# Kernel tuning notes

Hardware: AMD Instinct MI355X
Metric: run time of the kernel (lower is better)

## Reference

```python
import jax, jax.numpy as jnp
import numpy as np

B, R, IMG_DIM, TAG_DIM = 256, 36, 2048, 768
BOX_LEN = 15
POS_EMBED = 200
POS_SIZE = 16 * 16 + 1  # 257
EMBED_SIZE = 1024
EPS_NORM = 1e-8
EPS_ATTN = 1e-6


def setup_inputs() -> dict:
    key = jax.random.key(0)
    ks = jax.random.split(key, 8)
    images = jax.random.normal(ks[0], (B, R, IMG_DIM), dtype=jnp.float32)
    images_tag = jax.random.normal(ks[1], (B, R, TAG_DIM), dtype=jnp.float32)
    # boxes: first 15 entries are integer position indices, last 15 are weights
    box_idx = jax.random.randint(ks[2], (B, R, BOX_LEN), 0, POS_SIZE).astype(jnp.float32)
    box_w = jax.random.uniform(ks[3], (B, R, BOX_LEN), dtype=jnp.float32)
    boxes = jnp.concatenate([box_idx, box_w], axis=-1)  # [B,R,30]
    # parameters (xavier-uniform-like for linears, normal for embedding)
    pos_emb = jax.random.normal(ks[4], (POS_SIZE, POS_EMBED), dtype=jnp.float32)
    fan = (IMG_DIM + TAG_DIM) + POS_EMBED
    r1 = np.sqrt(6.0) / np.sqrt(fan)
    attn_W = jax.random.uniform(ks[5], (POS_EMBED, IMG_DIM + TAG_DIM), dtype=jnp.float32, minval=-r1, maxval=r1)
    fc_in = IMG_DIM + POS_EMBED + TAG_DIM
    r2 = np.sqrt(6.0) / np.sqrt(fc_in + EMBED_SIZE)
    fc_W = jax.random.uniform(ks[6], (EMBED_SIZE, fc_in), dtype=jnp.float32, minval=-r2, maxval=r2)
    fc_b = jnp.zeros((EMBED_SIZE,), dtype=jnp.float32)
    return {"images": images, "images_tag": images_tag, "boxes": boxes,
            "pos_emb": pos_emb, "attn_W": attn_W, "fc_W": fc_W, "fc_b": fc_b}


def reference(images, images_tag, boxes, pos_emb, attn_W, fc_W, fc_b):
    half = boxes.shape[2] // 2  # 15
    idx = boxes[..., :half].astype(jnp.int32)        # [B,R,15] position indices
    box_w = boxes[..., half:]                        # [B,R,15] weights
    img_tag = jnp.concatenate([images, images_tag], axis=-1)  # [B,R,2816]
    box_emb = pos_emb[idx]                           # [B,R,15,200]
    # posi_attn (vectorized over batch instead of python loop)
    region = jnp.einsum('brd,ed->bre', img_tag, attn_W)        # [B,R,200]
    scores = jnp.einsum('bre,brke->brk', region, box_emb)      # [B,R,15]
    attn = jax.nn.softmax(jnp.tanh(scores), axis=-1)
    attn = attn * box_w
    attn = attn / (jnp.sum(attn, axis=-1, keepdims=True) + EPS_ATTN)
    box_feat = jnp.einsum('brk,brke->bre', attn, box_emb)      # [B,R,200]
    # original uses .data -> detached attention output
    box_feat = jax.lax.stop_gradient(box_feat)
    image_position = jnp.concatenate([images, box_feat, images_tag], axis=-1)  # [B,R,3016]
    features = jnp.einsum('brd,ed->bre', image_position, fc_W) + fc_b
    norm = jnp.sqrt(jnp.sum(features ** 2, axis=-1, keepdims=True)) + EPS_NORM
    return features / norm
```

## Files before the change

### kernel.cpp

```cpp
#include <hip/hip_runtime.h>


#define M_TOT 9216
#define K1    2816
#define K2    3072
#define ES    1024

typedef __attribute__((ext_vector_type(8))) short bf16x8;
typedef __attribute__((ext_vector_type(4))) float floatx4;

static __device__ __forceinline__ unsigned short f2bf(float f) {
    unsigned int u = __float_as_uint(f);
    u += 0x7fffu + ((u >> 16) & 1u);
    return (unsigned short)(u >> 16);
}

static __device__ __forceinline__ void cvt8(const float* __restrict__ g,
                                            unsigned short* __restrict__ d) {
    const float4 f0 = *(const float4*)g;
    const float4 f1 = *(const float4*)(g + 4);
    uint4 pk;
    pk.x = (unsigned)f2bf(f0.x) | ((unsigned)f2bf(f0.y) << 16);
    pk.y = (unsigned)f2bf(f0.z) | ((unsigned)f2bf(f0.w) << 16);
    pk.z = (unsigned)f2bf(f1.x) | ((unsigned)f2bf(f1.y) << 16);
    pk.w = (unsigned)f2bf(f1.z) | ((unsigned)f2bf(f1.w) << 16);
    *(uint4*)d = pk;
}

static __device__ __forceinline__ void gl16(const void* g, const void* l) {
    __builtin_amdgcn_global_load_lds(
        (const __attribute__((address_space(1))) unsigned int*)g,
        (__attribute__((address_space(3))) unsigned int*)(unsigned int)(unsigned long long)l,
        16, 0, 0);
}

__global__ __launch_bounds__(384) void k_prep_a(
    const float* __restrict__ images,
    const float* __restrict__ tag,
    unsigned short* __restrict__ Abf)
{
    const int m = blockIdx.x;
    const int t = threadIdx.x;
    unsigned short* dst = Abf + (long)m * K2;
    if (t < 256) {
        cvt8(images + (long)m * 2048 + t * 8, dst + t * 8);
    } else if (t < 352) {
        const int j = t - 256;
        cvt8(tag + (long)m * 768 + j * 8, dst + 2304 + j * 8);
    }
}

__global__ __launch_bounds__(256) void k_prep_w(
    const float* __restrict__ attn_W,
    const float* __restrict__ fc_W,
    unsigned short* __restrict__ Wa,
    unsigned short* __restrict__ Wf)
{
    const int u = blockIdx.x * 256 + threadIdx.x;
    uint4 z; z.x = z.y = z.z = z.w = 0u;
    if (blockIdx.y == 0) {
        if (u < 208 * 352) {
            const int r = u / 352;
            const int c = (u - r * 352) * 8;
            if (r < 200) cvt8(attn_W + (long)r * K1 + c, Wa + (long)r * K1 + c);
            else         *(uint4*)(Wa + (long)r * K1 + c) = z;
        }
    } else {
        if (u < 1024 * 384) {
            const int r = u / 384;
            const int dc = (u - r * 384) * 8;
            unsigned short* d = Wf + (long)r * K2 + dc;
            if (dc < 2248)      cvt8(fc_W + (long)r * 3016 + dc, d);
            else if (dc < 2304) *(uint4*)d = z;
            else                cvt8(fc_W + (long)r * 3016 + (dc - 56), d);
        }
    }
}

__global__ __launch_bounds__(256, 2) void k_gemm1_attn(
    const unsigned short* __restrict__ Abf,
    const unsigned short* __restrict__ Wa,
    const float* __restrict__ boxes,
    const float* __restrict__ pos_emb,
    unsigned short* __restrict__ AbfBox)
{
    __shared__ __align__(16) unsigned short lds[14336];
    unsigned short* ldsA = lds;
    unsigned short* ldsB = lds + 1024;
    float* ldsR = (float*)lds;

    const int t = threadIdx.x;
    const int lane = t & 63;
    const int w = t >> 6;
    const int quad = lane >> 4;
    const int ln15 = lane & 15;
    const int x7 = ln15 & 7;
    const int m0 = blockIdx.x * 16;
    const int lrow = lane >> 3;
    const int schunk = (lane & 7) ^ lrow;
    const int nj = (w == 0) ? 4 : 3;

    floatx4 acc[4] = {};

    for (int kt = 0; kt < 44; ++kt) {
        const int kb = kt * 64;
        const int acol = kb + ((kb >= 2048) ? 256 : 0);
#pragma unroll
        for (int i = 0; i < 7; ++i) {
            const int u = w + i * 4;
            if (u < 26) {
                const int r = u * 8 + lrow;
                gl16(Wa + (long)r * K1 + kb + schunk * 8, ldsB + u * 512);
            } else {
                const int r = (u - 26) * 8 + lrow;
                gl16(Abf + (long)(m0 + r) * K2 + acol + schunk * 8,
                     ldsA + (u - 26) * 512);
            }
        }
        __syncthreads();
#pragma unroll
        for (int s = 0; s < 2; ++s) {
            const int g = s * 4 + quad;
            const int co = (g ^ x7) << 3;
            const bf16x8 a = *(const bf16x8*)&ldsA[ln15 * 64 + co];
#pragma unroll
            for (int jj = 0; jj < 4; ++jj) {
                if (jj < nj) {
                    const int j = w + jj * 4;
                    const bf16x8 b = *(const bf16x8*)&ldsB[(j * 16 + ln15) * 64 + co];
                    acc[jj] = __builtin_amdgcn_mfma_f32_16x16x32_bf16(a, b, acc[jj], 0, 0, 0);
                }
            }
        }
        __syncthreads();
    }

#pragma unroll
    for (int jj = 0; jj < 4; ++jj) {
        if (jj < nj) {
            const int j = w + jj * 4;
#pragma unroll
            for (int r = 0; r < 4; ++r)
                ldsR[(quad * 4 + r) * 212 + j * 16 + ln15] = acc[jj][r];
        }
    }
    __syncthreads();

    for (int rr = 0; rr < 4; ++rr) {
        const int ml = w * 4 + rr;
        const int m = m0 + ml;
        float rv[4];
#pragma unroll
        for (int c = 0; c < 4; ++c) {
            const int e = lane + c * 64;
            rv[c] = (e < 200) ? ldsR[ml * 212 + e] : 0.0f;
        }
        const float* bx = boxes + (long)m * 30;
        int idx[15]; float bw[15], sc[15];
#pragma unroll
        for (int k = 0; k < 15; ++k) {
            int ii = (int)bx[k];
            idx[k] = (ii < 0) ? 0 : (ii > 256 ? 256 : ii);
            bw[k] = bx[15 + k];
        }
#pragma unroll
        for (int k = 0; k < 15; ++k) {
            const float* em = pos_emb + (long)idx[k] * 200;
            float p = 0.0f;
#pragma unroll
            for (int c = 0; c < 4; ++c) {
                const int e = lane + c * 64;
                if (e < 200) p += rv[c] * em[e];
            }
            for (int off = 32; off; off >>= 1) p += __shfl_xor(p, off, 64);
            sc[k] = p;
        }
        float mx = -1e30f;
#pragma unroll
        for (int k = 0; k < 15; ++k) { sc[k] = tanhf(sc[k]); mx = fmaxf(mx, sc[k]); }
        float Z = 0.0f, den = 0.0f, pk[15];
#pragma unroll
        for (int k = 0; k < 15; ++k) { pk[k] = __expf(sc[k] - mx); Z += pk[k]; }
#pragma unroll
        for (int k = 0; k < 15; ++k) { pk[k] *= bw[k]; den += pk[k]; }
        den += 1e-6f * Z;
        const float inv = 1.0f / den;
        unsigned short* bo = AbfBox + (long)m * K2 + 2048;
#pragma unroll
        for (int c = 0; c < 4; ++c) {
            const int e = lane + c * 64;
            float o = 0.0f;
            if (e < 200) {
#pragma unroll
                for (int k = 0; k < 15; ++k) o += pk[k] * pos_emb[(long)idx[k] * 200 + e];
                o *= inv;
            }
            bo[e] = f2bf(o);
        }
    }
}

__global__ __launch_bounds__(256, 2) void k_gemm2(
    const unsigned short* __restrict__ Abf,
    const unsigned short* __restrict__ Wf,
    float* __restrict__ dout)
{
    __shared__ __align__(16) unsigned short ldsA[128 * 64];
    __shared__ __align__(16) unsigned short ldsB[128 * 64];
    const int t = threadIdx.x;
    const int lane = t & 63;
    const int w = t >> 6;
    const int quad = lane >> 4;
    const int ln15 = lane & 15;
    const int x7 = ln15 & 7;
    const int nx = blockIdx.x & 7;
    const int mx = blockIdx.x >> 3;
    const int m0 = mx * 128;
    const int n0 = nx * 128;
    const int lrow = lane >> 3;
    const int schunk = (lane & 7) ^ lrow;
    const int wm = (w & 1) * 64;
    const int wn = (w >> 1) * 64;

    floatx4 acc[4][4] = {};

    for (int kt = 0; kt < 48; ++kt) {
        const int kb = kt * 64;
#pragma unroll
        for (int i = 0; i < 4; ++i) {
            const int u = w * 4 + i;
            const int r = u * 8 + lrow;
            gl16(Abf + (long)(m0 + r) * K2 + kb + schunk * 8, ldsA + u * 512);
            gl16(Wf  + (long)(n0 + r) * K2 + kb + schunk * 8, ldsB + u * 512);
        }
        __syncthreads();
#pragma unroll
        for (int s = 0; s < 2; ++s) {
            const int g = s * 4 + quad;
            const int co = (g ^ x7) << 3;
            bf16x8 a[4], b[4];
#pragma unroll
            for (int i = 0; i < 4; ++i)
                a[i] = *(const bf16x8*)&ldsA[(wm + i * 16 + ln15) * 64 + co];
#pragma unroll
            for (int j = 0; j < 4; ++j)
                b[j] = *(const bf16x8*)&ldsB[(wn + j * 16 + ln15) * 64 + co];
#pragma unroll
            for (int i = 0; i < 4; ++i)
#pragma unroll
                for (int j = 0; j < 4; ++j)
                    acc[i][j] = __builtin_amdgcn_mfma_f32_16x16x32_bf16(a[i], b[j], acc[i][j], 0, 0, 0);
        }
        __syncthreads();
    }
#pragma unroll
    for (int i = 0; i < 4; ++i)
#pragma unroll
        for (int j = 0; j < 4; ++j) {
            const int row = m0 + wm + i * 16 + quad * 4;
            const int col = n0 + wn + j * 16 + ln15;
#pragma unroll
            for (int r = 0; r < 4; ++r)
                dout[(long)(row + r) * ES + col] = acc[i][j][r];
        }
}

__global__ __launch_bounds__(256) void k_norm(
    float* __restrict__ dout,
    const float* __restrict__ bias)
{
    __shared__ float red[4];
    const int m = blockIdx.x;
    const int t = threadIdx.x;
    float* f = dout + (long)m * ES + t * 4;
    float4 v = *(const float4*)f;
    const float4 bs = *(const float4*)(bias + t * 4);
    v.x += bs.x; v.y += bs.y; v.z += bs.z; v.w += bs.w;
    float ss = v.x * v.x + v.y * v.y + v.z * v.z + v.w * v.w;
    for (int off = 32; off; off >>= 1) ss += __shfl_xor(ss, off, 64);
    if ((t & 63) == 0) red[t >> 6] = ss;
    __syncthreads();
    const float total = red[0] + red[1] + red[2] + red[3];
    const float inv = 1.0f / (sqrtf(total) + 1e-8f);
    float4 o;
    o.x = v.x * inv; o.y = v.y * inv; o.z = v.z * inv; o.w = v.w * inv;
    *(float4*)f = o;
}

extern "C" void kernel_launch(void* const* d_in, const int* in_sizes, int n_in,
                              void* d_out, int out_size, void* d_ws, size_t ws_size,
                              hipStream_t stream) {
    const float* images  = (const float*)d_in[0];
    const float* tag     = (const float*)d_in[1];
    const float* boxes   = (const float*)d_in[2];
    const float* pos_emb = (const float*)d_in[3];
    const float* attn_W  = (const float*)d_in[4];
    const float* fc_W    = (const float*)d_in[5];
    const float* fc_b    = (const float*)d_in[6];
    float* out = (float*)d_out;

    unsigned short* Abf = (unsigned short*)d_ws;
    unsigned short* Wf  = Abf + (size_t)M_TOT * K2;
    unsigned short* Wa  = Wf  + (size_t)ES * K2;

    k_prep_a    <<<M_TOT, 384, 0, stream>>>(images, tag, Abf);
    k_prep_w    <<<dim3(1536, 2), 256, 0, stream>>>(attn_W, fc_W, Wa, Wf);
    k_gemm1_attn<<<576, 256, 0, stream>>>(Abf, Wa, boxes, pos_emb, Abf);
    k_gemm2     <<<576, 256, 0, stream>>>(Abf, Wf, out);
    k_norm      <<<M_TOT, 256, 0, stream>>>(out, fc_b);
}
```

Before: 333.5 us.

## Fuse activation bf16 conversion into gemm1 and retile gemm2 to 144x128

Removes the separate activation-conversion kernel: gemm1 now uses two extra waves that load fp32 images and tags, convert them to bf16 into LDS, and also write the bf16 copy to the workspace for gemm2. The Wa tile is no longer staged in LDS and is read directly from global memory in the MFMA loop, with the output columns split over 6 waves. gemm2 switches to 384-thread blocks on a 144x128 tile so its 512 blocks fit the CU count better. The weight prep kernel is flattened into a 1D grid. This trades a launch and a full pass over the activations for uncached direct global B loads and register-staged conversion inside the GEMM.

```diff
diff --git a/kernel.cpp b/kernel.cpp
--- a/kernel.cpp
+++ b/kernel.cpp
@@ -15,16 +15,18 @@
     return (unsigned short)(u >> 16);
 }
 
-static __device__ __forceinline__ void cvt8(const float* __restrict__ g,
-                                            unsigned short* __restrict__ d) {
-    const float4 f0 = *(const float4*)g;
-    const float4 f1 = *(const float4*)(g + 4);
+static __device__ __forceinline__ uint4 pack8(const float4 f0, const float4 f1) {
     uint4 pk;
     pk.x = (unsigned)f2bf(f0.x) | ((unsigned)f2bf(f0.y) << 16);
     pk.y = (unsigned)f2bf(f0.z) | ((unsigned)f2bf(f0.w) << 16);
     pk.z = (unsigned)f2bf(f1.x) | ((unsigned)f2bf(f1.y) << 16);
     pk.w = (unsigned)f2bf(f1.z) | ((unsigned)f2bf(f1.w) << 16);
-    *(uint4*)d = pk;
+    return pk;
+}
+
+static __device__ __forceinline__ void cvt8(const float* __restrict__ g,
+                                            unsigned short* __restrict__ d) {
+    *(uint4*)d = pack8(*(const float4*)g, *(const float4*)(g + 4));
 }
 
 static __device__ __forceinline__ void gl16(const void* g, const void* l) {
@@ -32,22 +34,6 @@
         (const __attribute__((address_space(1))) unsigned int*)g,
         (__attribute__((address_space(3))) unsigned int*)(unsigned int)(unsigned long long)l,
         16, 0, 0);
-}
-
-__global__ __launch_bounds__(384) void k_prep_a(
-    const float* __restrict__ images,
-    const float* __restrict__ tag,
-    unsigned short* __restrict__ Abf)
-{
-    const int m = blockIdx.x;
-    const int t = threadIdx.x;
-    unsigned short* dst = Abf + (long)m * K2;
-    if (t < 256) {
-        cvt8(images + (long)m * 2048 + t * 8, dst + t * 8);
-    } else if (t < 352) {
-        const int j = t - 256;
-        cvt8(tag + (long)m * 768 + j * 8, dst + 2304 + j * 8);
-    }
 }
 
 __global__ __launch_bounds__(256) void k_prep_w(
@@ -57,77 +43,85 @@
     unsigned short* __restrict__ Wf)
 {
     const int u = blockIdx.x * 256 + threadIdx.x;
+    const int NWF = 1024 * 384;
     uint4 z; z.x = z.y = z.z = z.w = 0u;
-    if (blockIdx.y == 0) {
-        if (u < 208 * 352) {
-            const int r = u / 352;
-            const int c = (u - r * 352) * 8;
+    if (u < NWF) {
+        const int r = u / 384;
+        const int dc = (u - r * 384) * 8;
+        unsigned short* d = Wf + (long)r * K2 + dc;
+        if (dc < 2248)      cvt8(fc_W + (long)r * 3016 + dc, d);
+        else if (dc < 2304) *(uint4*)d = z;
+        else                cvt8(fc_W + (long)r * 3016 + (dc - 56), d);
+    } else {
+        const int v = u - NWF;
+        if (v < 208 * 352) {
+            const int r = v / 352;
+            const int c = (v - r * 352) * 8;
             if (r < 200) cvt8(attn_W + (long)r * K1 + c, Wa + (long)r * K1 + c);
             else         *(uint4*)(Wa + (long)r * K1 + c) = z;
         }
-    } else {
-        if (u < 1024 * 384) {
-            const int r = u / 384;
-            const int dc = (u - r * 384) * 8;
-            unsigned short* d = Wf + (long)r * K2 + dc;
-            if (dc < 2248)      cvt8(fc_W + (long)r * 3016 + dc, d);
-            else if (dc < 2304) *(uint4*)d = z;
-            else                cvt8(fc_W + (long)r * 3016 + (dc - 56), d);
-        }
-    }
-}
-
-__global__ __launch_bounds__(256, 2) void k_gemm1_attn(
-    const unsigned short* __restrict__ Abf,
+    }
+}
+
+__global__ __launch_bounds__(384, 3) void k_gemm1_attn(
+    const float* __restrict__ images,
+    const float* __restrict__ tag,
     const unsigned short* __restrict__ Wa,
     const float* __restrict__ boxes,
     const float* __restrict__ pos_emb,
-    unsigned short* __restrict__ AbfBox)
+    unsigned short* __restrict__ Abf)
 {
-    __shared__ __align__(16) unsigned short lds[14336];
-    unsigned short* ldsA = lds;
-    unsigned short* ldsB = lds + 1024;
-    float* ldsR = (float*)lds;
+    __shared__ __align__(16) float ldsR[16][212];
+    unsigned short* ldsA = (unsigned short*)&ldsR[0][0];
 
     const int t = threadIdx.x;
     const int lane = t & 63;
     const int w = t >> 6;
     const int quad = lane >> 4;
     const int ln15 = lane & 15;
-    const int x7 = ln15 & 7;
+    const int x7 = ln15 & 15 & 7;
     const int m0 = blockIdx.x * 16;
-    const int lrow = lane >> 3;
-    const int schunk = (lane & 7) ^ lrow;
-    const int nj = (w == 0) ? 4 : 3;
-
-    floatx4 acc[4] = {};
+    const int nj = (w == 0) ? 3 : 2;
+
+    const bool stager = (t >= 256);
+    const int sr = (t - 256) >> 3;
+    const int sc = (t - 256) & 7;
+
+    floatx4 acc[3] = {};
+    float4 v0, v1;
+
+    if (stager) {
+        const float* src = images + (long)(m0 + sr) * 2048 + sc * 8;
+        v0 = *(const float4*)src;
+        v1 = *(const float4*)(src + 4);
+    }
 
     for (int kt = 0; kt < 44; ++kt) {
         const int kb = kt * 64;
-        const int acol = kb + ((kb >= 2048) ? 256 : 0);
-#pragma unroll
-        for (int i = 0; i < 7; ++i) {
-            const int u = w + i * 4;
-            if (u < 26) {
-                const int r = u * 8 + lrow;
-                gl16(Wa + (long)r * K1 + kb + schunk * 8, ldsB + u * 512);
-            } else {
-                const int r = (u - 26) * 8 + lrow;
-                gl16(Abf + (long)(m0 + r) * K2 + acol + schunk * 8,
-                     ldsA + (u - 26) * 512);
-            }
+        if (stager) {
+            const uint4 pk = pack8(v0, v1);
+            *(uint4*)&ldsA[sr * 64 + ((sc ^ (sr & 7)) << 3)] = pk;
+            const int acol = kb + ((kb >= 2048) ? 256 : 0);
+            *(uint4*)(Abf + (long)(m0 + sr) * K2 + acol + sc * 8) = pk;
         }
         __syncthreads();
+        if (stager && kt < 43) {
+            const int kn = kb + 64;
+            const float* src = (kn < 2048)
+                ? images + (long)(m0 + sr) * 2048 + kn + sc * 8
+                : tag + (long)(m0 + sr) * 768 + (kn - 2048) + sc * 8;
+            v0 = *(const float4*)src;
+            v1 = *(const float4*)(src + 4);
+        }
 #pragma unroll
         for (int s = 0; s < 2; ++s) {
             const int g = s * 4 + quad;
-            const int co = (g ^ x7) << 3;
-            const bf16x8 a = *(const bf16x8*)&ldsA[ln15 * 64 + co];
-#pragma unroll
-            for (int jj = 0; jj < 4; ++jj) {
+            const bf16x8 a = *(const bf16x8*)&ldsA[ln15 * 64 + ((g ^ x7) << 3)];
+#pragma unroll
+            for (int jj = 0; jj < 3; ++jj) {
                 if (jj < nj) {
-                    const int j = w + jj * 4;
-                    const bf16x8 b = *(const bf16x8*)&ldsB[(j * 16 + ln15) * 64 + co];
+                    const int j = w + jj * 6;
+                    const bf16x8 b = *(const bf16x8*)(Wa + (long)(j * 16 + ln15) * K1 + kb + g * 8);
                     acc[jj] = __builtin_amdgcn_mfma_f32_16x16x32_bf16(a, b, acc[jj], 0, 0, 0);
                 }
             }
@@ -136,27 +130,28 @@
     }
 
 #pragma unroll
-    for (int jj = 0; jj < 4; ++jj) {
+    for (int jj = 0; jj < 3; ++jj) {
         if (jj < nj) {
-            const int j = w + jj * 4;
+            const int j = w + jj * 6;
 #pragma unroll
             for (int r = 0; r < 4; ++r)
-                ldsR[(quad * 4 + r) * 212 + j * 16 + ln15] = acc[jj][r];
+                ldsR[quad * 4 + r][j * 16 + ln15] = acc[jj][r];
         }
     }
     __syncthreads();
 
-    for (int rr = 0; rr < 4; ++rr) {
-        const int ml = w * 4 + rr;
+    for (int rr = 0; rr < 3; ++rr) {
+        const int ml = w + rr * 6;
+        if (ml >= 16) break;
         const int m = m0 + ml;
         float rv[4];
 #pragma unroll
         for (int c = 0; c < 4; ++c) {
             const int e = lane + c * 64;
-            rv[c] = (e < 200) ? ldsR[ml * 212 + e] : 0.0f;
+            rv[c] = (e < 200) ? ldsR[ml][e] : 0.0f;
         }
         const float* bx = boxes + (long)m * 30;
-        int idx[15]; float bw[15], sc[15];
+        int idx[15]; float bw[15], sc_[15];
 #pragma unroll
         for (int k = 0; k < 15; ++k) {
             int ii = (int)bx[k];
@@ -173,19 +168,19 @@
                 if (e < 200) p += rv[c] * em[e];
             }
             for (int off = 32; off; off >>= 1) p += __shfl_xor(p, off, 64);
-            sc[k] = p;
+            sc_[k] = p;
         }
         float mx = -1e30f;
 #pragma unroll
-        for (int k = 0; k < 15; ++k) { sc[k] = tanhf(sc[k]); mx = fmaxf(mx, sc[k]); }
+        for (int k = 0; k < 15; ++k) { sc_[k] = tanhf(sc_[k]); mx = fmaxf(mx, sc_[k]); }
         float Z = 0.0f, den = 0.0f, pk[15];
 #pragma unroll
-        for (int k = 0; k < 15; ++k) { pk[k] = __expf(sc[k] - mx); Z += pk[k]; }
+        for (int k = 0; k < 15; ++k) { pk[k] = __expf(sc_[k] - mx); Z += pk[k]; }
 #pragma unroll
         for (int k = 0; k < 15; ++k) { pk[k] *= bw[k]; den += pk[k]; }
         den += 1e-6f * Z;
         const float inv = 1.0f / den;
-        unsigned short* bo = AbfBox + (long)m * K2 + 2048;
+        unsigned short* bo = Abf + (long)m * K2 + 2048;
 #pragma unroll
         for (int c = 0; c < 4; ++c) {
             const int e = lane + c * 64;
@@ -200,12 +195,12 @@
     }
 }
 
-__global__ __launch_bounds__(256, 2) void k_gemm2(
+__global__ __launch_bounds__(384, 3) void k_gemm2(
     const unsigned short* __restrict__ Abf,
     const unsigned short* __restrict__ Wf,
     float* __restrict__ dout)
 {
-    __shared__ __align__(16) unsigned short ldsA[128 * 64];
+    __shared__ __align__(16) unsigned short ldsA[144 * 64];
     __shared__ __align__(16) unsigned short ldsB[128 * 64];
     const int t = threadIdx.x;
     const int lane = t & 63;
@@ -215,38 +210,41 @@
     const int x7 = ln15 & 7;
     const int nx = blockIdx.x & 7;
     const int mx = blockIdx.x >> 3;
-    const int m0 = mx * 128;
+    const int m0 = mx * 144;
     const int n0 = nx * 128;
     const int lrow = lane >> 3;
     const int schunk = (lane & 7) ^ lrow;
-    const int wm = (w & 1) * 64;
-    const int wn = (w >> 1) * 64;
-
-    floatx4 acc[4][4] = {};
+    const int wm = (w % 3) * 48;
+    const int wn = (w / 3) * 64;
+
+    floatx4 acc[3][4] = {};
 
     for (int kt = 0; kt < 48; ++kt) {
         const int kb = kt * 64;
 #pragma unroll
-        for (int i = 0; i < 4; ++i) {
-            const int u = w * 4 + i;
-            const int r = u * 8 + lrow;
-            gl16(Abf + (long)(m0 + r) * K2 + kb + schunk * 8, ldsA + u * 512);
-            gl16(Wf  + (long)(n0 + r) * K2 + kb + schunk * 8, ldsB + u * 512);
+        for (int i = 0; i < 6; ++i) {
+            const int u = w + i * 6;
+            if (u < 18) {
+                gl16(Abf + (long)(m0 + u * 8 + lrow) * K2 + kb + schunk * 8, ldsA + u * 512);
+            } else if (u < 34) {
+                gl16(Wf + (long)(n0 + (u - 18) * 8 + lrow) * K2 + kb + schunk * 8,
+                     ldsB + (u - 18) * 512);
+            }
         }
         __syncthreads();
 #pragma unroll
         for (int s = 0; s < 2; ++s) {
             const int g = s * 4 + quad;
             const int co = (g ^ x7) << 3;
-            bf16x8 a[4], b[4];
-#pragma unroll
-            for (int i = 0; i < 4; ++i)
+            bf16x8 a[3], b[4];
+#pragma unroll
+            for (int i = 0; i < 3; ++i)
                 a[i] = *(const bf16x8*)&ldsA[(wm + i * 16 + ln15) * 64 + co];
 #pragma unroll
             for (int j = 0; j < 4; ++j)
                 b[j] = *(const bf16x8*)&ldsB[(wn + j * 16 + ln15) * 64 + co];
 #pragma unroll
-            for (int i = 0; i < 4; ++i)
+            for (int i = 0; i < 3; ++i)
 #pragma unroll
                 for (int j = 0; j < 4; ++j)
                     acc[i][j] = __builtin_amdgcn_mfma_f32_16x16x32_bf16(a[i], b[j], acc[i][j], 0, 0, 0);
@@ -254,7 +252,7 @@
         __syncthreads();
     }
 #pragma unroll
-    for (int i = 0; i < 4; ++i)
+    for (int i = 0; i < 3; ++i)
 #pragma unroll
         for (int j = 0; j < 4; ++j) {
             const int row = m0 + wm + i * 16 + quad * 4;
@@ -303,9 +301,8 @@
     unsigned short* Wf  = Abf + (size_t)M_TOT * K2;
     unsigned short* Wa  = Wf  + (size_t)ES * K2;
 
-    k_prep_a    <<<M_TOT, 384, 0, stream>>>(images, tag, Abf);
-    k_prep_w    <<<dim3(1536, 2), 256, 0, stream>>>(attn_W, fc_W, Wa, Wf);
-    k_gemm1_attn<<<576, 256, 0, stream>>>(Abf, Wa, boxes, pos_emb, Abf);
-    k_gemm2     <<<576, 256, 0, stream>>>(Abf, Wf, out);
+    k_prep_w    <<<1822, 256, 0, stream>>>(attn_W, fc_W, Wa, Wf);
+    k_gemm1_attn<<<576, 384, 0, stream>>>(images, tag, Wa, boxes, pos_emb, Abf);
+    k_gemm2     <<<512, 384, 0, stream>>>(Abf, Wf, out);
     k_norm      <<<M_TOT, 256, 0, stream>>>(out, fc_b);
 }
```

Result: slower. 421.6 us (+26.4%).

## Merge prep kernels, raise occupancy hints, and remap gemm2 grid to 2D

Applied to the files above, without the earlier changes.

Combines the activation and weight bf16-conversion kernels into one flat-indexed kernel, eliminating a launch and idle threads. Raises launch_bounds min-blocks from 2 to 4 on both GEMM kernels to push more waves per CU, at the risk of register spilling. Changes the gemm2 block ordering so M varies fastest across blocks, which alters L2/cache reuse of A vs weight tiles.

```diff
diff --git a/kernel.cpp b/kernel.cpp
--- a/kernel.cpp
+++ b/kernel.cpp
@@ -34,50 +34,44 @@
         16, 0, 0);
 }
 
-__global__ __launch_bounds__(384) void k_prep_a(
+#define NC_ABF (9216 * 352)
+#define NC_WF  (1024 * 384)
+#define NC_WA  ( 208 * 352)
+__global__ __launch_bounds__(256) void k_prep(
     const float* __restrict__ images,
     const float* __restrict__ tag,
-    unsigned short* __restrict__ Abf)
-{
-    const int m = blockIdx.x;
-    const int t = threadIdx.x;
-    unsigned short* dst = Abf + (long)m * K2;
-    if (t < 256) {
-        cvt8(images + (long)m * 2048 + t * 8, dst + t * 8);
-    } else if (t < 352) {
-        const int j = t - 256;
-        cvt8(tag + (long)m * 768 + j * 8, dst + 2304 + j * 8);
-    }
-}
-
-__global__ __launch_bounds__(256) void k_prep_w(
     const float* __restrict__ attn_W,
     const float* __restrict__ fc_W,
+    unsigned short* __restrict__ Abf,
     unsigned short* __restrict__ Wa,
     unsigned short* __restrict__ Wf)
 {
     const int u = blockIdx.x * 256 + threadIdx.x;
     uint4 z; z.x = z.y = z.z = z.w = 0u;
-    if (blockIdx.y == 0) {
-        if (u < 208 * 352) {
-            const int r = u / 352;
-            const int c = (u - r * 352) * 8;
-            if (r < 200) cvt8(attn_W + (long)r * K1 + c, Wa + (long)r * K1 + c);
-            else         *(uint4*)(Wa + (long)r * K1 + c) = z;
-        }
-    } else {
-        if (u < 1024 * 384) {
-            const int r = u / 384;
-            const int dc = (u - r * 384) * 8;
-            unsigned short* d = Wf + (long)r * K2 + dc;
-            if (dc < 2248)      cvt8(fc_W + (long)r * 3016 + dc, d);
-            else if (dc < 2304) *(uint4*)d = z;
-            else                cvt8(fc_W + (long)r * 3016 + (dc - 56), d);
-        }
-    }
-}
-
-__global__ __launch_bounds__(256, 2) void k_gemm1_attn(
+    if (u < NC_ABF) {
+        const int m = u / 352;
+        const int c = u - m * 352;
+        if (c < 256) cvt8(images + (long)m * 2048 + c * 8, Abf + (long)m * K2 + c * 8);
+        else         cvt8(tag + (long)m * 768 + (c - 256) * 8,
+                          Abf + (long)m * K2 + 2304 + (c - 256) * 8);
+    } else if (u < NC_ABF + NC_WF) {
+        const int v = u - NC_ABF;
+        const int r = v / 384;
+        const int dc = (v - r * 384) * 8;
+        unsigned short* d = Wf + (long)r * K2 + dc;
+        if (dc < 2248)      cvt8(fc_W + (long)r * 3016 + dc, d);
+        else if (dc < 2304) *(uint4*)d = z;
+        else                cvt8(fc_W + (long)r * 3016 + (dc - 56), d);
+    } else if (u < NC_ABF + NC_WF + NC_WA) {
+        const int v = u - NC_ABF - NC_WF;
+        const int r = v / 352;
+        const int c = (v - r * 352) * 8;
+        if (r < 200) cvt8(attn_W + (long)r * K1 + c, Wa + (long)r * K1 + c);
+        else         *(uint4*)(Wa + (long)r * K1 + c) = z;
+    }
+}
+
+__global__ __launch_bounds__(256, 4) void k_gemm1_attn(
     const unsigned short* __restrict__ Abf,
     const unsigned short* __restrict__ Wa,
     const float* __restrict__ boxes,
@@ -156,7 +150,7 @@
             rv[c] = (e < 200) ? ldsR[ml * 212 + e] : 0.0f;
         }
         const float* bx = boxes + (long)m * 30;
-        int idx[15]; float bw[15], sc[15];
+        int idx[15]; float bw[15], sc_[15];
 #pragma unroll
         for (int k = 0; k < 15; ++k) {
             int ii = (int)bx[k];
@@ -173,14 +167,14 @@
                 if (e < 200) p += rv[c] * em[e];
             }
             for (int off = 32; off; off >>= 1) p += __shfl_xor(p, off, 64);
-            sc[k] = p;
+            sc_[k] = p;
         }
         float mx = -1e30f;
 #pragma unroll
-        for (int k = 0; k < 15; ++k) { sc[k] = tanhf(sc[k]); mx = fmaxf(mx, sc[k]); }
+        for (int k = 0; k < 15; ++k) { sc_[k] = tanhf(sc_[k]); mx = fmaxf(mx, sc_[k]); }
         float Z = 0.0f, den = 0.0f, pk[15];
 #pragma unroll
-        for (int k = 0; k < 15; ++k) { pk[k] = __expf(sc[k] - mx); Z += pk[k]; }
+        for (int k = 0; k < 15; ++k) { pk[k] = __expf(sc_[k] - mx); Z += pk[k]; }
 #pragma unroll
         for (int k = 0; k < 15; ++k) { pk[k] *= bw[k]; den += pk[k]; }
         den += 1e-6f * Z;
@@ -200,7 +194,7 @@
     }
 }
 
-__global__ __launch_bounds__(256, 2) void k_gemm2(
+__global__ __launch_bounds__(256, 4) void k_gemm2(
     const unsigned short* __restrict__ Abf,
     const unsigned short* __restrict__ Wf,
     float* __restrict__ dout)
@@ -213,10 +207,8 @@
     const int quad = lane >> 4;
     const int ln15 = lane & 15;
     const int x7 = ln15 & 7;
-    const int nx = blockIdx.x & 7;
-    const int mx = blockIdx.x >> 3;
-    const int m0 = mx * 128;
-    const int n0 = nx * 128;
+    const int m0 = blockIdx.x * 128;
+    const int n0 = blockIdx.y * 128;
     const int lrow = lane >> 3;
     const int schunk = (lane & 7) ^ lrow;
     const int wm = (w & 1) * 64;
@@ -303,9 +295,9 @@
     unsigned short* Wf  = Abf + (size_t)M_TOT * K2;
     unsigned short* Wa  = Wf  + (size_t)ES * K2;
 
-    k_prep_a    <<<M_TOT, 384, 0, stream>>>(images, tag, Abf);
-    k_prep_w    <<<dim3(1536, 2), 256, 0, stream>>>(attn_W, fc_W, Wa, Wf);
+    const int prep_blocks = (NC_ABF + NC_WF + NC_WA + 255) / 256;
+    k_prep      <<<prep_blocks, 256, 0, stream>>>(images, tag, attn_W, fc_W, Abf, Wa, Wf);
     k_gemm1_attn<<<576, 256, 0, stream>>>(Abf, Wa, boxes, pos_emb, Abf);
-    k_gemm2     <<<576, 256, 0, stream>>>(Abf, Wf, out);
+    k_gemm2     <<<dim3(72, 8), 256, 0, stream>>>(Abf, Wf, out);
     k_norm      <<<M_TOT, 256, 0, stream>>>(out, fc_b);
 }
```

Result: faster. 316.0 us (-5.3%).
